# Performance work log

Measured on AMD Instinct MI355X. Metric: run time of the kernel, lower is better.

Reference implementation:

```python
import jax, jax.numpy as jnp
import numpy as np

EMB_DIM = 2048
HIDDEN_DIM = 8192
BATCH = 4
SEQ = 2048


def _kaiming_normal(key, out_f, in_f):
    # kaiming_normal_(mode='fan_in', nonlinearity='relu'): std = sqrt(2 / fan_in)
    std = np.sqrt(2.0 / in_f).astype(np.float32)
    return jax.random.normal(key, (out_f, in_f), dtype=jnp.float32) * std


def setup_inputs() -> dict:
    key = jax.random.key(0)
    kx, k1, k2, k3 = jax.random.split(key, 4)
    x = jax.random.normal(kx, (BATCH, SEQ, EMB_DIM), dtype=jnp.float32)
    w1 = _kaiming_normal(k1, HIDDEN_DIM, EMB_DIM)   # fc1.weight [hidden, emb]
    w2 = _kaiming_normal(k2, HIDDEN_DIM, EMB_DIM)   # fc2.weight [hidden, emb]
    w3 = _kaiming_normal(k3, EMB_DIM, HIDDEN_DIM)   # fc3.weight [emb, hidden]
    return {"x": x, "w1": w1, "w2": w2, "w3": w3, "scale_x": 1}


def reference(x, w1, w2, w3, scale_x):
    # fc1/fc2: x @ W.T  (no bias). scale_x is unused in the fp (calibration) path.
    gate = jnp.einsum('bse,he->bsh', x, w1)  # [B,S,H]
    up = jnp.einsum('bse,he->bsh', x, w2)    # [B,S,H]
    h = jax.nn.silu(gate) * up               # Custom_SiLU + Custom_ElementWiseMul
    out = jnp.einsum('bsh,eh->bse', h, w3)   # fc3 down-projection
    return out
```

## Files before the change

kernel.cpp:

```cpp
#include <hip/hip_runtime.h>
#include <hip/hip_bf16.h>

#define M_ROWS 8192
#define E_DIM  2048
#define H_DIM  8192

typedef __attribute__((ext_vector_type(8))) short bf16x8;
typedef __attribute__((ext_vector_type(4))) float f32x4;
typedef __attribute__((ext_vector_type(4))) unsigned int uint4v;

__device__ __forceinline__ unsigned short f2bf_rne(float x) {
  unsigned u = __builtin_bit_cast(unsigned, x);
  u += 0x7FFFu + ((u >> 16) & 1u);
  return (unsigned short)(u >> 16);
}

__device__ __forceinline__ float bf2f(unsigned short b) {
  unsigned u = ((unsigned)b) << 16;
  return __builtin_bit_cast(float, u);
}

__global__ __launch_bounds__(256) void cvt4_f32_bf16(const float* __restrict__ s0, unsigned short* __restrict__ d0,
                                                     const float* __restrict__ s1, unsigned short* __restrict__ d1,
                                                     const float* __restrict__ s2, unsigned short* __restrict__ d2,
                                                     const float* __restrict__ s3, unsigned short* __restrict__ d3,
                                                     int n8) {
  int i = blockIdx.x * blockDim.x + threadIdx.x;
  if (i >= n8) return;
  const float* in = (blockIdx.y == 0) ? s0 : (blockIdx.y == 1) ? s1 : (blockIdx.y == 2) ? s2 : s3;
  unsigned short* out = (blockIdx.y == 0) ? d0 : (blockIdx.y == 1) ? d1 : (blockIdx.y == 2) ? d2 : d3;
  const float4* p = (const float4*)(in + (size_t)i * 8);
  float4 a = p[0];
  float4 b = p[1];
  union { unsigned short us[8]; uint4v v; } r;
  r.us[0] = f2bf_rne(a.x); r.us[1] = f2bf_rne(a.y);
  r.us[2] = f2bf_rne(a.z); r.us[3] = f2bf_rne(a.w);
  r.us[4] = f2bf_rne(b.x); r.us[5] = f2bf_rne(b.y);
  r.us[6] = f2bf_rne(b.z); r.us[7] = f2bf_rne(b.w);
  *(uint4v*)(out + (size_t)i * 8) = r.v;
}

__device__ __forceinline__ void gld_lds16(const unsigned short* g, unsigned short* l) {
  __builtin_amdgcn_global_load_lds(
      (const __attribute__((address_space(1))) unsigned int*)g,
      (__attribute__((address_space(3))) unsigned int*)l, 16, 0, 0);
}

#define VMCNT(n)   asm volatile("s_waitcnt vmcnt(" #n ")" ::: "memory")

template <int EPI>
__global__ __launch_bounds__(512, 2)
void gemm256(const unsigned short* __restrict__ A,
             const unsigned short* __restrict__ B,
             const unsigned short* __restrict__ B2,
             void* __restrict__ Cout,
             int M, int N, int K) {
  __shared__ unsigned short sh[65536];
  unsigned short* lAb = sh;
  unsigned short* lBb = sh + 32768;

  const int tid = threadIdx.x;
  const int lane = tid & 63;
  const int wave = tid >> 6;
  const int wr = wave >> 2;
  const int wc = wave & 3;
  const int lr = lane & 15, lk = lane >> 4;

  const int gx = gridDim.x;
  const int wg = blockIdx.y * gx + blockIdx.x;
  int bcol, brow;
  if constexpr (EPI == 3) {
    const int xcd = wg & 7, idx = wg >> 3;
    bcol = xcd * 8 + (idx & 7);
    brow = idx >> 3;
  } else {
    const int nwg = gx * gridDim.y;
    const int swz = (wg & 7) * (nwg >> 3) + (wg >> 3);
    bcol = swz % gx;
    brow = swz / gx;
  }

  const unsigned short* Ag = A + (size_t)brow * 256 * K;
  const unsigned short* BgH0;
  const unsigned short* BgH1;
  if constexpr (EPI == 3) {
    BgH0 = B  + (size_t)bcol * 128 * K;
    BgH1 = B2 + (size_t)bcol * 128 * K;
  } else {
    BgH0 = B + (size_t)bcol * 256 * K;
    BgH1 = BgH0 + (size_t)128 * K;
  }

  f32x4 acc[8][4] = {};
  const int NT = K >> 6;
  const int NI = NT >> 1;

  auto stageH = [&](const unsigned short* gbase, unsigned short* ldsh) {
#pragma unroll
    for (int i = 0; i < 2; ++i) {
      int p = i * 4096 + tid * 8;
      int row = p >> 6;
      int lslot = ((p >> 3) & 7) ^ (row & 7);
      gld_lds16(gbase + (size_t)row * K + lslot * 8, ldsh + p);
    }
  };

  const int xsw = (lr & 7) << 3;
  bf16x8 af[8][2], bf[4][2];

#define RD_A(MLO, SRC) \
  _Pragma("unroll") for (int m = MLO; m < MLO + 4; ++m) { \
    int r = wr * 128 + m * 16 + lr; \
    af[m][0] = *(const bf16x8*)&SRC[(r * 64 + lk * 8) ^ xsw]; \
    af[m][1] = *(const bf16x8*)&SRC[(r * 64 + 32 + lk * 8) ^ xsw]; }
#define RD_B(NLO, SRC) \
  _Pragma("unroll") for (int n = NLO; n < NLO + 2; ++n) { \
    int r = wc * 64 + n * 16 + lr; \
    bf[n][0] = *(const bf16x8*)&SRC[(r * 64 + lk * 8) ^ xsw]; \
    bf[n][1] = *(const bf16x8*)&SRC[(r * 64 + 32 + lk * 8) ^ xsw]; }
#define PH_MFMA(MLO, NLO) \
  __builtin_amdgcn_s_barrier(); \
  asm volatile("s_waitcnt lgkmcnt(0)" ::: "memory"); \
  __builtin_amdgcn_sched_barrier(0); \
  __builtin_amdgcn_s_setprio(1); \
  _Pragma("unroll") for (int m = MLO; m < MLO + 4; ++m) \
  _Pragma("unroll") for (int n = NLO; n < NLO + 2; ++n) \
  _Pragma("unroll") for (int ks = 0; ks < 2; ++ks) \
    acc[m][n] = __builtin_amdgcn_mfma_f32_16x16x32_bf16(af[m][ks], bf[n][ks], acc[m][n], 0, 0, 0); \
  __builtin_amdgcn_s_setprio(0);

  stageH(Ag, lAb);
  stageH(Ag + (size_t)128 * K, lAb + 8192);
  stageH(BgH0, lBb);
  stageH(BgH1, lBb + 8192);
  stageH(Ag + 64, lAb + 16384);
  stageH(Ag + (size_t)128 * K + 64, lAb + 16384 + 8192);
  stageH(BgH0 + 64, lBb + 16384);
  stageH(BgH1 + 64, lBb + 16384 + 8192);
  VMCNT(0);
  __builtin_amdgcn_s_barrier();

  const unsigned short* lA0 = lAb;
  const unsigned short* lB0 = lBb;
  const unsigned short* lA1 = lAb + 16384;
  const unsigned short* lB1 = lBb + 16384;

  for (int it = 0; it < NI; ++it) {
    const int t = it << 1;
    const size_t kT1 = (size_t)(t + 1) * 64;
    const size_t kS2 = (size_t)((t + 2 < NT) ? t + 2 : NT - 1) * 64;
    const size_t kS3 = (size_t)((t + 3 < NT) ? t + 3 : NT - 1) * 64;

    RD_A(0, lA0); RD_B(0, lB0);
    if (it > 0) stageH(Ag + (size_t)128 * K + kT1, lAb + 16384 + 8192);
    asm volatile("s_waitcnt lgkmcnt(8)" ::: "memory");
    PH_MFMA(0, 0);
    __builtin_amdgcn_s_barrier();

    RD_B(2, lB0);
    PH_MFMA(0, 2);
    __builtin_amdgcn_s_barrier();

    RD_A(4, lA0);
    stageH(BgH0 + kS2, lBb);
    PH_MFMA(4, 0);
    __builtin_amdgcn_s_barrier();

    stageH(BgH1 + kS2, lBb + 8192);
    stageH(Ag + kS2, lAb);
    PH_MFMA(4, 2);
    VMCNT(6);
    __builtin_amdgcn_s_barrier();

    RD_A(0, lA1); RD_B(0, lB1);
    stageH(Ag + (size_t)128 * K + kS2, lAb + 8192);
    asm volatile("s_waitcnt lgkmcnt(8)" ::: "memory");
    PH_MFMA(0, 0);
    __builtin_amdgcn_s_barrier();

    RD_B(2, lB1);
    PH_MFMA(0, 2);
    __builtin_amdgcn_s_barrier();

    RD_A(4, lA1);
    stageH(BgH0 + kS3, lBb + 16384);
    PH_MFMA(4, 0);
    __builtin_amdgcn_s_barrier();

    stageH(BgH1 + kS3, lBb + 16384 + 8192);
    stageH(Ag + kS3, lAb + 16384);
    PH_MFMA(4, 2);
    VMCNT(6);
    __builtin_amdgcn_s_barrier();
  }
  VMCNT(0);

#undef RD_A
#undef RD_B
#undef PH_MFMA

  if constexpr (EPI == 3) {
    __builtin_amdgcn_s_barrier();
    if (wc >= 2) {
      float* rg = (float*)(sh + (wr * 2 + (wc - 2)) * 16384);
#pragma unroll
      for (int m = 0; m < 8; ++m)
#pragma unroll
        for (int n = 0; n < 4; ++n)
#pragma unroll
          for (int j = 0; j < 4; ++j)
            rg[(m * 16 + n * 4 + j) * 64 + lane] = acc[m][n][j];
    }
    asm volatile("s_waitcnt lgkmcnt(0)" ::: "memory");
    __builtin_amdgcn_s_barrier();
    if (wc < 2) {
      const float* rg = (const float*)(sh + (wr * 2 + wc) * 16384);
      const int row0 = brow * 256 + wr * 128 + lk * 4;
      const int col0 = bcol * 128 + wc * 64 + lr;
#pragma unroll
      for (int m = 0; m < 8; ++m)
#pragma unroll
        for (int n = 0; n < 4; ++n)
#pragma unroll
          for (int j = 0; j < 4; ++j) {
            float g = acc[m][n][j];
            float u = rg[(m * 16 + n * 4 + j) * 64 + lane];
            float s = g / (1.0f + __expf(-g));
            ((unsigned short*)Cout)[(size_t)(row0 + m * 16 + j) * N + (col0 + n * 16)] =
                f2bf_rne(s * u);
          }
    }
  } else {
    const int row0 = brow * 256 + wr * 128 + lk * 4;
    const int col0 = bcol * 256 + wc * 64 + lr;
#pragma unroll
    for (int m = 0; m < 8; ++m)
#pragma unroll
      for (int n = 0; n < 4; ++n)
#pragma unroll
        for (int j = 0; j < 4; ++j) {
          size_t idx = (size_t)(row0 + m * 16 + j) * N + (col0 + n * 16);
          ((float*)Cout)[idx] = acc[m][n][j];
        }
  }
}

extern "C" void kernel_launch(void* const* d_in, const int* in_sizes, int n_in,
                              void* d_out, int out_size, void* d_ws, size_t ws_size,
                              hipStream_t stream) {
  const float* x  = (const float*)d_in[0];
  const float* w1 = (const float*)d_in[1];
  const float* w2 = (const float*)d_in[2];
  const float* w3 = (const float*)d_in[3];
  float* out = (float*)d_out;

  const int M = M_ROWS, E = E_DIM, H = H_DIM;

  unsigned short* xb  = (unsigned short*)d_ws;
  unsigned short* w1b = xb + (size_t)M * E;
  unsigned short* w2b = w1b + (size_t)H * E;
  unsigned short* hb  = w2b + (size_t)H * E;

  const int n8 = (M * E) / 8;
  const size_t need_hoist = ((size_t)M * E + 2 * (size_t)H * E + (size_t)M * H + (size_t)E * H) * 2;

  if (ws_size >= need_hoist) {
    unsigned short* w3b = hb + (size_t)M * H;
    cvt4_f32_bf16<<<dim3(n8 / 256, 4), 256, 0, stream>>>(x, xb, w1, w1b, w2, w2b, w3, w3b, n8);
    gemm256<3><<<dim3(H / 128, M / 256), 512, 0, stream>>>(xb, w1b, w2b, hb, M, H, E);
    gemm256<0><<<dim3(E / 256, M / 256), 512, 0, stream>>>(hb, w3b, nullptr, out, M, E, H);
  } else {
    unsigned short* w3b = xb;
    cvt4_f32_bf16<<<dim3(n8 / 256, 3), 256, 0, stream>>>(x, xb, w1, w1b, w2, w2b, nullptr, nullptr, n8);
    gemm256<3><<<dim3(H / 128, M / 256), 512, 0, stream>>>(xb, w1b, w2b, hb, M, H, E);
    cvt4_f32_bf16<<<dim3(n8 / 256, 1), 256, 0, stream>>>(w3, w3b, nullptr, nullptr, nullptr, nullptr, nullptr, nullptr, n8);
    gemm256<0><<<dim3(E / 256, M / 256), 512, 0, stream>>>(hb, w3b, nullptr, out, M, E, H);
  }
}
```

Measured before the change: 823.5 us.

## Remap fused gate/up GEMM waves so each wave holds matching gate and up accumulators

For the fused gate/up kernel, waves are remapped to a 4x2 grid. Each wave now computes a 64x64 output tile for both gate and up, keeping them in accumulators 0-3 and 4-7 and reading the up weights from a separate LDS region. This removes the epilogue exchange through LDS, with its extra barriers and shared-memory traffic, because SiLU*up can be done directly in registers. The change alters the LDS read pattern, since A fragments are reused across the gate and up B fragments, and it adds another fragment array (bu), which may raise register pressure.

```diff
diff --git a/kernel.cpp b/kernel.cpp
--- a/kernel.cpp
+++ b/kernel.cpp
@@ -13,11 +13,6 @@
   unsigned u = __builtin_bit_cast(unsigned, x);
   u += 0x7FFFu + ((u >> 16) & 1u);
   return (unsigned short)(u >> 16);
-}
-
-__device__ __forceinline__ float bf2f(unsigned short b) {
-  unsigned u = ((unsigned)b) << 16;
-  return __builtin_bit_cast(float, u);
 }
 
 __global__ __launch_bounds__(256) void cvt4_f32_bf16(const float* __restrict__ s0, unsigned short* __restrict__ d0,
@@ -64,6 +59,8 @@
   const int wave = tid >> 6;
   const int wr = wave >> 2;
   const int wc = wave & 3;
+  const int wrow = wave >> 1;
+  const int wcol = wave & 1;
   const int lr = lane & 15, lk = lane >> 4;
 
   const int gx = gridDim.x;
@@ -106,28 +103,74 @@
   };
 
   const int xsw = (lr & 7) << 3;
-  bf16x8 af[8][2], bf[4][2];
-
-#define RD_A(MLO, SRC) \
-  _Pragma("unroll") for (int m = MLO; m < MLO + 4; ++m) { \
-    int r = wr * 128 + m * 16 + lr; \
-    af[m][0] = *(const bf16x8*)&SRC[(r * 64 + lk * 8) ^ xsw]; \
-    af[m][1] = *(const bf16x8*)&SRC[(r * 64 + 32 + lk * 8) ^ xsw]; }
-#define RD_B(NLO, SRC) \
-  _Pragma("unroll") for (int n = NLO; n < NLO + 2; ++n) { \
-    int r = wc * 64 + n * 16 + lr; \
-    bf[n][0] = *(const bf16x8*)&SRC[(r * 64 + lk * 8) ^ xsw]; \
-    bf[n][1] = *(const bf16x8*)&SRC[(r * 64 + 32 + lk * 8) ^ xsw]; }
-#define PH_MFMA(MLO, NLO) \
+  bf16x8 af[8][2], bf[4][2], bu[4][2];
+
+#define RD_PH1(LA, LB) \
+  if constexpr (EPI == 3) { \
+    _Pragma("unroll") for (int m = 0; m < 4; ++m) { \
+      int r = wrow * 64 + m * 16 + lr; \
+      af[m][0] = *(const bf16x8*)&LA[(r * 64 + lk * 8) ^ xsw]; \
+      af[m][1] = *(const bf16x8*)&LA[(r * 64 + 32 + lk * 8) ^ xsw]; } \
+    _Pragma("unroll") for (int n = 0; n < 2; ++n) { \
+      int r = wcol * 64 + n * 16 + lr; \
+      bf[n][0] = *(const bf16x8*)&LB[(r * 64 + lk * 8) ^ xsw]; \
+      bf[n][1] = *(const bf16x8*)&LB[(r * 64 + 32 + lk * 8) ^ xsw]; } \
+  } else { \
+    _Pragma("unroll") for (int m = 0; m < 4; ++m) { \
+      int r = wr * 128 + m * 16 + lr; \
+      af[m][0] = *(const bf16x8*)&LA[(r * 64 + lk * 8) ^ xsw]; \
+      af[m][1] = *(const bf16x8*)&LA[(r * 64 + 32 + lk * 8) ^ xsw]; } \
+    _Pragma("unroll") for (int n = 0; n < 2; ++n) { \
+      int r = wc * 64 + n * 16 + lr; \
+      bf[n][0] = *(const bf16x8*)&LB[(r * 64 + lk * 8) ^ xsw]; \
+      bf[n][1] = *(const bf16x8*)&LB[(r * 64 + 32 + lk * 8) ^ xsw]; } \
+  }
+#define RD_PH2(LB) \
+  if constexpr (EPI == 3) { \
+    _Pragma("unroll") for (int n = 2; n < 4; ++n) { \
+      int r = wcol * 64 + n * 16 + lr; \
+      bf[n][0] = *(const bf16x8*)&LB[(r * 64 + lk * 8) ^ xsw]; \
+      bf[n][1] = *(const bf16x8*)&LB[(r * 64 + 32 + lk * 8) ^ xsw]; } \
+  } else { \
+    _Pragma("unroll") for (int n = 2; n < 4; ++n) { \
+      int r = wc * 64 + n * 16 + lr; \
+      bf[n][0] = *(const bf16x8*)&LB[(r * 64 + lk * 8) ^ xsw]; \
+      bf[n][1] = *(const bf16x8*)&LB[(r * 64 + 32 + lk * 8) ^ xsw]; } \
+  }
+#define RD_PH3(LA, LB) \
+  if constexpr (EPI == 3) { \
+    _Pragma("unroll") for (int n = 0; n < 4; ++n) { \
+      int r = wcol * 64 + n * 16 + lr; \
+      bu[n][0] = *(const bf16x8*)&LB[8192 + ((r * 64 + lk * 8) ^ xsw)]; \
+      bu[n][1] = *(const bf16x8*)&LB[8192 + ((r * 64 + 32 + lk * 8) ^ xsw)]; } \
+  } else { \
+    _Pragma("unroll") for (int m = 4; m < 8; ++m) { \
+      int r = wr * 128 + m * 16 + lr; \
+      af[m][0] = *(const bf16x8*)&LA[(r * 64 + lk * 8) ^ xsw]; \
+      af[m][1] = *(const bf16x8*)&LA[(r * 64 + 32 + lk * 8) ^ xsw]; } \
+  }
+#define PH_CORE_BEGIN \
   __builtin_amdgcn_s_barrier(); \
   asm volatile("s_waitcnt lgkmcnt(0)" ::: "memory"); \
   __builtin_amdgcn_sched_barrier(0); \
-  __builtin_amdgcn_s_setprio(1); \
-  _Pragma("unroll") for (int m = MLO; m < MLO + 4; ++m) \
-  _Pragma("unroll") for (int n = NLO; n < NLO + 2; ++n) \
-  _Pragma("unroll") for (int ks = 0; ks < 2; ++ks) \
-    acc[m][n] = __builtin_amdgcn_mfma_f32_16x16x32_bf16(af[m][ks], bf[n][ks], acc[m][n], 0, 0, 0); \
-  __builtin_amdgcn_s_setprio(0);
+  __builtin_amdgcn_s_setprio(1);
+#define PH_CORE_END __builtin_amdgcn_s_setprio(0);
+#define MF(ACC_M, AV, BV) \
+  acc[ACC_M][n] = __builtin_amdgcn_mfma_f32_16x16x32_bf16(AV[ks], BV[ks], acc[ACC_M][n], 0, 0, 0);
+#define PH_MFMA_Q(Q) \
+  PH_CORE_BEGIN \
+  if constexpr (EPI == 3) { \
+    if constexpr (Q == 1) { _Pragma("unroll") for (int m = 0; m < 4; ++m) _Pragma("unroll") for (int n = 0; n < 2; ++n) _Pragma("unroll") for (int ks = 0; ks < 2; ++ks) MF(m, af[m], bf[n]) } \
+    if constexpr (Q == 2) { _Pragma("unroll") for (int m = 0; m < 4; ++m) _Pragma("unroll") for (int n = 2; n < 4; ++n) _Pragma("unroll") for (int ks = 0; ks < 2; ++ks) MF(m, af[m], bf[n]) } \
+    if constexpr (Q == 3) { _Pragma("unroll") for (int m = 0; m < 4; ++m) _Pragma("unroll") for (int n = 0; n < 2; ++n) _Pragma("unroll") for (int ks = 0; ks < 2; ++ks) MF(m + 4, af[m], bu[n]) } \
+    if constexpr (Q == 4) { _Pragma("unroll") for (int m = 0; m < 4; ++m) _Pragma("unroll") for (int n = 2; n < 4; ++n) _Pragma("unroll") for (int ks = 0; ks < 2; ++ks) MF(m + 4, af[m], bu[n]) } \
+  } else { \
+    if constexpr (Q == 1) { _Pragma("unroll") for (int m = 0; m < 4; ++m) _Pragma("unroll") for (int n = 0; n < 2; ++n) _Pragma("unroll") for (int ks = 0; ks < 2; ++ks) MF(m, af[m], bf[n]) } \
+    if constexpr (Q == 2) { _Pragma("unroll") for (int m = 0; m < 4; ++m) _Pragma("unroll") for (int n = 2; n < 4; ++n) _Pragma("unroll") for (int ks = 0; ks < 2; ++ks) MF(m, af[m], bf[n]) } \
+    if constexpr (Q == 3) { _Pragma("unroll") for (int m = 4; m < 8; ++m) _Pragma("unroll") for (int n = 0; n < 2; ++n) _Pragma("unroll") for (int ks = 0; ks < 2; ++ks) MF(m, af[m], bf[n]) } \
+    if constexpr (Q == 4) { _Pragma("unroll") for (int m = 4; m < 8; ++m) _Pragma("unroll") for (int n = 2; n < 4; ++n) _Pragma("unroll") for (int ks = 0; ks < 2; ++ks) MF(m, af[m], bf[n]) } \
+  } \
+  PH_CORE_END
 
   stageH(Ag, lAb);
   stageH(Ag + (size_t)128 * K, lAb + 8192);
@@ -151,85 +194,73 @@
     const size_t kS2 = (size_t)((t + 2 < NT) ? t + 2 : NT - 1) * 64;
     const size_t kS3 = (size_t)((t + 3 < NT) ? t + 3 : NT - 1) * 64;
 
-    RD_A(0, lA0); RD_B(0, lB0);
+    RD_PH1(lA0, lB0);
     if (it > 0) stageH(Ag + (size_t)128 * K + kT1, lAb + 16384 + 8192);
     asm volatile("s_waitcnt lgkmcnt(8)" ::: "memory");
-    PH_MFMA(0, 0);
-    __builtin_amdgcn_s_barrier();
-
-    RD_B(2, lB0);
-    PH_MFMA(0, 2);
-    __builtin_amdgcn_s_barrier();
-
-    RD_A(4, lA0);
+    PH_MFMA_Q(1);
+    __builtin_amdgcn_s_barrier();
+
+    RD_PH2(lB0);
+    PH_MFMA_Q(2);
+    __builtin_amdgcn_s_barrier();
+
+    RD_PH3(lA0, lB0);
     stageH(BgH0 + kS2, lBb);
-    PH_MFMA(4, 0);
+    PH_MFMA_Q(3);
     __builtin_amdgcn_s_barrier();
 
     stageH(BgH1 + kS2, lBb + 8192);
     stageH(Ag + kS2, lAb);
-    PH_MFMA(4, 2);
+    PH_MFMA_Q(4);
     VMCNT(6);
     __builtin_amdgcn_s_barrier();
 
-    RD_A(0, lA1); RD_B(0, lB1);
+    RD_PH1(lA1, lB1);
     stageH(Ag + (size_t)128 * K + kS2, lAb + 8192);
     asm volatile("s_waitcnt lgkmcnt(8)" ::: "memory");
-    PH_MFMA(0, 0);
-    __builtin_amdgcn_s_barrier();
-
-    RD_B(2, lB1);
-    PH_MFMA(0, 2);
-    __builtin_amdgcn_s_barrier();
-
-    RD_A(4, lA1);
+    PH_MFMA_Q(1);
+    __builtin_amdgcn_s_barrier();
+
+    RD_PH2(lB1);
+    PH_MFMA_Q(2);
+    __builtin_amdgcn_s_barrier();
+
+    RD_PH3(lA1, lB1);
     stageH(BgH0 + kS3, lBb + 16384);
-    PH_MFMA(4, 0);
+    PH_MFMA_Q(3);
     __builtin_amdgcn_s_barrier();
 
     stageH(BgH1 + kS3, lBb + 16384 + 8192);
     stageH(Ag + kS3, lAb + 16384);
-    PH_MFMA(4, 2);
+    PH_MFMA_Q(4);
     VMCNT(6);
     __builtin_amdgcn_s_barrier();
   }
   VMCNT(0);
 
-#undef RD_A
-#undef RD_B
-#undef PH_MFMA
+#undef RD_PH1
+#undef RD_PH2
+#undef RD_PH3
+#undef PH_CORE_BEGIN
+#undef PH_CORE_END
+#undef MF
+#undef PH_MFMA_Q
 
   if constexpr (EPI == 3) {
-    __builtin_amdgcn_s_barrier();
-    if (wc >= 2) {
-      float* rg = (float*)(sh + (wr * 2 + (wc - 2)) * 16384);
-#pragma unroll
-      for (int m = 0; m < 8; ++m)
-#pragma unroll
-        for (int n = 0; n < 4; ++n)
-#pragma unroll
-          for (int j = 0; j < 4; ++j)
-            rg[(m * 16 + n * 4 + j) * 64 + lane] = acc[m][n][j];
-    }
-    asm volatile("s_waitcnt lgkmcnt(0)" ::: "memory");
-    __builtin_amdgcn_s_barrier();
-    if (wc < 2) {
-      const float* rg = (const float*)(sh + (wr * 2 + wc) * 16384);
-      const int row0 = brow * 256 + wr * 128 + lk * 4;
-      const int col0 = bcol * 128 + wc * 64 + lr;
-#pragma unroll
-      for (int m = 0; m < 8; ++m)
-#pragma unroll
-        for (int n = 0; n < 4; ++n)
-#pragma unroll
-          for (int j = 0; j < 4; ++j) {
-            float g = acc[m][n][j];
-            float u = rg[(m * 16 + n * 4 + j) * 64 + lane];
-            float s = g / (1.0f + __expf(-g));
-            ((unsigned short*)Cout)[(size_t)(row0 + m * 16 + j) * N + (col0 + n * 16)] =
-                f2bf_rne(s * u);
-          }
-    }
+    const int row0 = brow * 256 + wrow * 64 + lk * 4;
+    const int col0 = bcol * 128 + wcol * 64 + lr;
+#pragma unroll
+    for (int m = 0; m < 4; ++m)
+#pragma unroll
+      for (int n = 0; n < 4; ++n)
+#pragma unroll
+        for (int j = 0; j < 4; ++j) {
+          float g = acc[m][n][j];
+          float u = acc[m + 4][n][j];
+          float s = g / (1.0f + __expf(-g));
+          ((unsigned short*)Cout)[(size_t)(row0 + m * 16 + j) * N + (col0 + n * 16)] =
+              f2bf_rne(s * u);
+        }
   } else {
     const int row0 = brow * 256 + wr * 128 + lk * 4;
     const int col0 = bcol * 256 + wc * 64 + lr;
```

Measured after the change: 768.1 us. -6.7%, faster.
